# Performance work log

Measured on AMD Instinct MI355X. Metric: run time of the kernel, lower is better.

## Reference

```python
import jax, jax.numpy as jnp
import numpy as np

DEC_LEN = 64  # matches init_kwargs dec_len
B, T = 64, 8192


def setup_inputs() -> dict:
    key = jax.random.key(0)
    k1, k2, k3, k4 = jax.random.split(key, 4)
    return {
        "feats_in": jax.random.normal(k1, (B, T, 1), jnp.float32),
        "X_in": jax.random.normal(k2, (B, T, 1), jnp.float32),
        "feats_out": jax.random.normal(k3, (B, DEC_LEN, 1), jnp.float32),
        "X_out": jax.random.normal(k4, (B, DEC_LEN, 1), jnp.float32),
    }


def reference(feats_in, X_in, feats_out, X_out):
    L = DEC_LEN
    n_win = X_in.shape[1] - L            # number of sliding windows (T - dec_len)
    x = X_in[..., 0]                     # [B, T]
    y = X_out[..., 0]                    # [B, L]
    # all sliding windows via gather: [n_win, L] index -> [B, n_win, L]
    win_idx = jnp.arange(n_win)[:, None] + jnp.arange(L)[None, :]
    windows = x[:, win_idx]              # [B, n_win, L]
    # per-window mean squared distance to the target window
    dists = jnp.mean((windows - y[:, None, :]) ** 2, axis=2)  # [B, n_win]
    start = jnp.argmin(dists, axis=1)    # [B]
    gidx = start[:, None] + jnp.arange(L)[None, :]            # [B, L]
    mean_out = jnp.take_along_axis(x, gidx, axis=1)[..., None]  # [B, L, 1]
    return mean_out
```

## Files before the change

kernel.cpp:

```cpp
#include <hip/hip_runtime.h>

constexpr int B_SZ  = 64;
constexpr int T_SZ  = 8192;
constexpr int L_SZ  = 64;
constexpr int NWIN  = T_SZ - L_SZ;
constexpr int NQ    = 8;
constexpr int QW    = NWIN / NQ;
constexpr int STAGE = QW + L_SZ;

__global__ __launch_bounds__(256)
void window_match_fused(const float* __restrict__ X_in,
                        const float* __restrict__ X_out,
                        unsigned long long* __restrict__ ws_keys,
                        unsigned int* __restrict__ ws_cnt,
                        float* __restrict__ out)
{
    __shared__ float xs[STAGE + 8];
    __shared__ float ys[L_SZ];
    __shared__ unsigned long long wred[4];
    __shared__ int s_win;

    const int bq  = blockIdx.x;
    const int b   = bq >> 3;
    const int q   = bq & 7;
    const int tid = threadIdx.x;
    const int base = q * QW;

    const float4* xg  = reinterpret_cast<const float4*>(X_in + (size_t)b * T_SZ + base);
    float4*       xs4 = reinterpret_cast<float4*>(xs);
    for (int i = tid; i < STAGE / 4; i += 256)
        xs4[i] = xg[i];

    if (tid < L_SZ) ys[tid] = X_out[(size_t)b * L_SZ + tid];
    __syncthreads();

    float y[L_SZ];
    #pragma unroll
    for (int j = 0; j < L_SZ; ++j) y[j] = ys[j];

    unsigned long long best = ~0ull;

    const int s0 = 4 * tid;
    if (s0 < QW) {
        float xv[68];
        const float4* p = reinterpret_cast<const float4*>(xs + s0);
        #pragma unroll
        for (int i = 0; i < 17; ++i) {
            float4 v = p[i];
            xv[4 * i + 0] = v.x;
            xv[4 * i + 1] = v.y;
            xv[4 * i + 2] = v.z;
            xv[4 * i + 3] = v.w;
        }
        #pragma unroll
        for (int w = 0; w < 4; ++w) {
            float d = 0.0f;
            #pragma unroll
            for (int j = 0; j < L_SZ; ++j) {
                const float t = xv[w + j] - y[j];
                d = fmaf(t, t, d);
            }
            const unsigned long long key =
                ((unsigned long long)__float_as_uint(d) << 32) |
                (unsigned int)(base + s0 + w);
            best = key < best ? key : best;
        }
    }

    #pragma unroll
    for (int off = 32; off > 0; off >>= 1) {
        const unsigned long long o = __shfl_down(best, off, 64);
        best = o < best ? o : best;
    }
    if ((tid & 63) == 0) wred[tid >> 6] = best;
    __syncthreads();

    if (tid == 0) {
        unsigned long long m = wred[0];
        m = wred[1] < m ? wred[1] : m;
        m = wred[2] < m ? wred[2] : m;
        m = wred[3] < m ? wred[3] : m;

        __hip_atomic_store(&ws_keys[bq], m, __ATOMIC_RELEASE,
                           __HIP_MEMORY_SCOPE_AGENT);
        const unsigned int old = __hip_atomic_fetch_add(&ws_cnt[b], 1u,
                                                        __ATOMIC_ACQ_REL,
                                                        __HIP_MEMORY_SCOPE_AGENT);
        int sw = -1;
        if ((old & 7u) == 7u) {
            unsigned long long g = __hip_atomic_load(&ws_keys[b * NQ + 0],
                                                     __ATOMIC_ACQUIRE,
                                                     __HIP_MEMORY_SCOPE_AGENT);
            #pragma unroll
            for (int qq = 1; qq < NQ; ++qq) {
                const unsigned long long o = __hip_atomic_load(&ws_keys[b * NQ + qq],
                                                               __ATOMIC_ACQUIRE,
                                                               __HIP_MEMORY_SCOPE_AGENT);
                g = o < g ? o : g;
            }
            sw = (int)(g & 0xffffffffu);
        }
        s_win = sw;
    }
    __syncthreads();

    const int s = s_win;
    if (s >= 0 && tid < L_SZ)
        out[(size_t)b * L_SZ + tid] = X_in[(size_t)b * T_SZ + s + tid];
}

extern "C" void kernel_launch(void* const* d_in, const int* in_sizes, int n_in,
                              void* d_out, int out_size, void* d_ws, size_t ws_size,
                              hipStream_t stream) {
    const float* X_in  = (const float*)d_in[1];
    const float* X_out = (const float*)d_in[3];
    float* out = (float*)d_out;
    unsigned long long* ws_keys = (unsigned long long*)d_ws;
    unsigned int* ws_cnt = (unsigned int*)((char*)d_ws + B_SZ * NQ * 8);

    window_match_fused<<<B_SZ * NQ, 256, 0, stream>>>(X_in, X_out, ws_keys, ws_cnt, out);
}
```

Baseline: 79.48 us.

## Use one workgroup per batch row with full-row LDS staging

Replaces the eight-way split per batch row and the cross-block atomic reduction with a single 512-thread workgroup per row. The whole row is staged in swizzled LDS, and each thread scans 16 consecutive windows. This removes global atomics and workspace traffic and improves register reuse of loaded x values. In exchange the grid shrinks to 64 workgroups, which leaves much of the GPU idle.

```diff
diff --git a/kernel.cpp b/kernel.cpp
--- a/kernel.cpp
+++ b/kernel.cpp
@@ -1,59 +1,56 @@
 #include <hip/hip_runtime.h>
 
-constexpr int B_SZ  = 64;
-constexpr int T_SZ  = 8192;
-constexpr int L_SZ  = 64;
-constexpr int NWIN  = T_SZ - L_SZ;
-constexpr int NQ    = 8;
-constexpr int QW    = NWIN / NQ;
-constexpr int STAGE = QW + L_SZ;
+constexpr int B_SZ = 64;
+constexpr int T_SZ = 8192;
+constexpr int L_SZ = 64;
+constexpr int NWIN = T_SZ - L_SZ;
+constexpr int NTHR = 512;
+constexpr int WPT  = 16;
 
-__global__ __launch_bounds__(256)
-void window_match_fused(const float* __restrict__ X_in,
-                        const float* __restrict__ X_out,
-                        unsigned long long* __restrict__ ws_keys,
-                        unsigned int* __restrict__ ws_cnt,
-                        float* __restrict__ out)
+__device__ __forceinline__ int swz(int i) { return i ^ ((i >> 3) & 7); }
+
+__global__ __launch_bounds__(NTHR, 2)
+void window_match_one(const float* __restrict__ X_in,
+                      const float* __restrict__ X_out,
+                      float* __restrict__ out)
 {
-    __shared__ float xs[STAGE + 8];
-    __shared__ float ys[L_SZ];
-    __shared__ unsigned long long wred[4];
+    __shared__ float xs[T_SZ];
+    __shared__ float ysh[L_SZ];
+    __shared__ unsigned long long wred[NTHR / 64];
     __shared__ int s_win;
 
-    const int bq  = blockIdx.x;
-    const int b   = bq >> 3;
-    const int q   = bq & 7;
+    const int b   = blockIdx.x;
     const int tid = threadIdx.x;
-    const int base = q * QW;
 
-    const float4* xg  = reinterpret_cast<const float4*>(X_in + (size_t)b * T_SZ + base);
+    const float4* xg  = reinterpret_cast<const float4*>(X_in + (size_t)b * T_SZ);
     float4*       xs4 = reinterpret_cast<float4*>(xs);
-    for (int i = tid; i < STAGE / 4; i += 256)
-        xs4[i] = xg[i];
-
-    if (tid < L_SZ) ys[tid] = X_out[(size_t)b * L_SZ + tid];
+    #pragma unroll
+    for (int r = 0; r < T_SZ / 4 / NTHR; ++r) {
+        const int i = tid + r * NTHR;
+        xs4[swz(i)] = xg[i];
+    }
+    if (tid < L_SZ) ysh[tid] = X_out[(size_t)b * L_SZ + tid];
     __syncthreads();
 
     float y[L_SZ];
     #pragma unroll
-    for (int j = 0; j < L_SZ; ++j) y[j] = ys[j];
+    for (int j = 0; j < L_SZ; ++j) y[j] = ysh[j];
 
     unsigned long long best = ~0ull;
-
-    const int s0 = 4 * tid;
-    if (s0 < QW) {
-        float xv[68];
-        const float4* p = reinterpret_cast<const float4*>(xs + s0);
+    const int s0 = WPT * tid;
+    if (s0 < NWIN) {
+        float xv[WPT + L_SZ];
+        const float4* xr = reinterpret_cast<const float4*>(xs);
         #pragma unroll
-        for (int i = 0; i < 17; ++i) {
-            float4 v = p[i];
+        for (int i = 0; i < (WPT + L_SZ) / 4; ++i) {
+            const float4 v = xr[swz(4 * tid + i)];
             xv[4 * i + 0] = v.x;
             xv[4 * i + 1] = v.y;
             xv[4 * i + 2] = v.z;
             xv[4 * i + 3] = v.w;
         }
         #pragma unroll
-        for (int w = 0; w < 4; ++w) {
+        for (int w = 0; w < WPT; ++w) {
             float d = 0.0f;
             #pragma unroll
             for (int j = 0; j < L_SZ; ++j) {
@@ -62,7 +59,7 @@
             }
             const unsigned long long key =
                 ((unsigned long long)__float_as_uint(d) << 32) |
-                (unsigned int)(base + s0 + w);
+                (unsigned int)(s0 + w);
             best = key < best ? key : best;
         }
     }
@@ -77,36 +74,17 @@
 
     if (tid == 0) {
         unsigned long long m = wred[0];
-        m = wred[1] < m ? wred[1] : m;
-        m = wred[2] < m ? wred[2] : m;
-        m = wred[3] < m ? wred[3] : m;
-
-        __hip_atomic_store(&ws_keys[bq], m, __ATOMIC_RELEASE,
-                           __HIP_MEMORY_SCOPE_AGENT);
-        const unsigned int old = __hip_atomic_fetch_add(&ws_cnt[b], 1u,
-                                                        __ATOMIC_ACQ_REL,
-                                                        __HIP_MEMORY_SCOPE_AGENT);
-        int sw = -1;
-        if ((old & 7u) == 7u) {
-            unsigned long long g = __hip_atomic_load(&ws_keys[b * NQ + 0],
-                                                     __ATOMIC_ACQUIRE,
-                                                     __HIP_MEMORY_SCOPE_AGENT);
-            #pragma unroll
-            for (int qq = 1; qq < NQ; ++qq) {
-                const unsigned long long o = __hip_atomic_load(&ws_keys[b * NQ + qq],
-                                                               __ATOMIC_ACQUIRE,
-                                                               __HIP_MEMORY_SCOPE_AGENT);
-                g = o < g ? o : g;
-            }
-            sw = (int)(g & 0xffffffffu);
+        #pragma unroll
+        for (int wv = 1; wv < NTHR / 64; ++wv) {
+            const unsigned long long o = wred[wv];
+            m = o < m ? o : m;
         }
-        s_win = sw;
+        s_win = (int)(m & 0xffffffffu);
     }
     __syncthreads();
 
-    const int s = s_win;
-    if (s >= 0 && tid < L_SZ)
-        out[(size_t)b * L_SZ + tid] = X_in[(size_t)b * T_SZ + s + tid];
+    if (tid < L_SZ)
+        out[(size_t)b * L_SZ + tid] = X_in[(size_t)b * T_SZ + s_win + tid];
 }
 
 extern "C" void kernel_launch(void* const* d_in, const int* in_sizes, int n_in,
@@ -115,8 +93,6 @@
     const float* X_in  = (const float*)d_in[1];
     const float* X_out = (const float*)d_in[3];
     float* out = (float*)d_out;
-    unsigned long long* ws_keys = (unsigned long long*)d_ws;
-    unsigned int* ws_cnt = (unsigned int*)((char*)d_ws + B_SZ * NQ * 8);
 
-    window_match_fused<<<B_SZ * NQ, 256, 0, stream>>>(X_in, X_out, ws_keys, ws_cnt, out);
+    window_match_one<<<B_SZ, NTHR, 0, stream>>>(X_in, X_out, out);
 }
```

Measured after the change: 88.84 us. 11.8% more time.
